# Optimization experiments

Measured on AMD Instinct MI355X. Metric: run time of the kernel, lower is better.

## Reference

```python
import jax, jax.numpy as jnp
import numpy as np
import math

D_MODEL = 1024
HEADS = 16
D_K = D_MODEL // HEADS
D_FF = 2048
EPS = 1e-6
NEG = -1e9


def _layernorm(x, gamma, beta):
    mu = x.mean(axis=-1, keepdims=True)
    var = ((x - mu) ** 2).mean(axis=-1, keepdims=True)
    return gamma * (x - mu) / jnp.sqrt(var + EPS) + beta


def setup_inputs() -> dict:
    key = jax.random.key(0)
    ks = jax.random.split(key, 12)
    B, S = 8, 1024
    s = 0.02
    return {
        "x": jax.random.normal(ks[0], (B, S, D_MODEL), jnp.float32),
        "mask": jnp.ones((B, 1, S), jnp.int32),
        "wq": jax.random.normal(ks[1], (D_MODEL, D_MODEL), jnp.float32) * s,
        "bq": jnp.zeros((D_MODEL,), jnp.float32),
        "wk": jax.random.normal(ks[2], (D_MODEL, D_MODEL), jnp.float32) * s,
        "bk": jnp.zeros((D_MODEL,), jnp.float32),
        "wv": jax.random.normal(ks[3], (D_MODEL, D_MODEL), jnp.float32) * s,
        "bv": jnp.zeros((D_MODEL,), jnp.float32),
        "wo": jax.random.normal(ks[4], (D_MODEL, D_MODEL), jnp.float32) * s,
        "bo": jnp.zeros((D_MODEL,), jnp.float32),
        "w1": jax.random.normal(ks[5], (D_MODEL, D_FF), jnp.float32) * s,
        "b1": jnp.zeros((D_FF,), jnp.float32),
        "w2": jax.random.normal(ks[6], (D_FF, D_MODEL), jnp.float32) * s,
        "b2": jnp.zeros((D_MODEL,), jnp.float32),
        "g1": jnp.ones((D_MODEL,), jnp.float32),
        "be1": jnp.zeros((D_MODEL,), jnp.float32),
        "g2": jnp.ones((D_MODEL,), jnp.float32),
        "be2": jnp.zeros((D_MODEL,), jnp.float32),
    }


def reference(x, mask, wq, bq, wk, bk, wv, bv, wo, bo, w1, b1, w2, b2, g1, be1, g2, be2):
    B, S, _ = x.shape
    # QKV projections, split heads: [B,H,S,d_k]
    q = (x @ wq + bq).reshape(B, S, HEADS, D_K).transpose(0, 2, 1, 3)
    k = (x @ wk + bk).reshape(B, S, HEADS, D_K).transpose(0, 2, 1, 3)
    v = (x @ wv + bv).reshape(B, S, HEADS, D_K).transpose(0, 2, 1, 3)
    scores = jnp.einsum("bhqd,bhkd->bhqk", q, k) / math.sqrt(D_K)
    m = mask[:, None, :, :]  # [B,1,1|S,S] broadcast over heads
    scores = jnp.where(m == 0, NEG, scores)
    attn = jax.nn.softmax(scores, axis=-1)
    out = jnp.einsum("bhqk,bhkd->bhqd", attn, v)
    concat = out.transpose(0, 2, 1, 3).reshape(B, S, D_MODEL)
    attn_out = concat @ wo + bo
    x1 = _layernorm(x + attn_out, g1, be1)
    ff = jax.nn.relu(x1 @ w1 + b1) @ w2 + b2
    return _layernorm(x1 + ff, g2, be2)
```

## Files before the change

kernel.cpp:

```cpp
#include <hip/hip_runtime.h>
#include <stdint.h>

using u16 = unsigned short;
using u32 = unsigned int;
typedef __attribute__((ext_vector_type(4))) float f32x4;
typedef __attribute__((ext_vector_type(8))) short s16x8;

#define LOG2E 1.44269504088896340736f
#define SCL (0.125f * LOG2E)

__device__ __forceinline__ u16 f2b(float f) {
  union { float f; u32 u; } v; v.f = f;
  u32 r = v.u + 0x7fffu + ((v.u >> 16) & 1u);
  return (u16)(r >> 16);
}

__device__ __forceinline__ float b2f(u16 x) {
  union { u32 u; float f; } v; v.u = (u32)x << 16; return v.f;
}

__device__ __forceinline__ u32 pack2(u16 lo, u16 hi) {
  return (u32)lo | ((u32)hi << 16);
}

__device__ __forceinline__ u32 cvtpk(float lo, float hi) {
  u32 r;
  asm("v_cvt_pk_bf16_f32 %0, %1, %2" : "=v"(r) : "v"(lo), "v"(hi));
  return r;
}

__device__ __forceinline__ float fexp2(float x) {
  float t = fmaf(x, 8388608.f, 1065053744.f);
  t = fmaxf(t, 0.f);
  union { u32 u; float f; } v; v.u = (u32)t;
  return v.f;
}

__device__ __forceinline__ f32x4 mfma16(s16x8 a, s16x8 b, f32x4 c) {
  return __builtin_amdgcn_mfma_f32_16x16x32_bf16(a, b, c, 0, 0, 0);
}

__device__ __forceinline__ void gload16(const void* g, void* l) {
  __builtin_amdgcn_global_load_lds(
      (const __attribute__((address_space(1))) void*)g,
      (__attribute__((address_space(3))) void*)l, 16, 0, 0);
}

__global__ __launch_bounds__(256) void cvt_bf16(const float* __restrict__ in,
                                                u16* __restrict__ out, int n4) {
  int i = blockIdx.x * 256 + threadIdx.x;
  if (i >= n4) return;
  float4 v = ((const float4*)in)[i];
  uint2 o;
  o.x = pack2(f2b(v.x), f2b(v.y));
  o.y = pack2(f2b(v.z), f2b(v.w));
  ((uint2*)out)[i] = o;
}

__global__ __launch_bounds__(256) void transpose_cvt(const float* __restrict__ in,
                                                     u16* __restrict__ outT,
                                                     int K, int N) {
  __shared__ float t[32][33];
  int n0 = blockIdx.x * 32, k0 = blockIdx.y * 32;
  int tx = threadIdx.x, ty = threadIdx.y;
#pragma unroll
  for (int i = 0; i < 4; i++)
    t[ty + i * 8][tx] = in[(size_t)(k0 + ty + i * 8) * N + n0 + tx];
  __syncthreads();
#pragma unroll
  for (int i = 0; i < 4; i++)
    outT[(size_t)(n0 + ty + i * 8) * K + k0 + tx] = f2b(t[tx][ty + i * 8]);
}

__global__ __launch_bounds__(256) void bias_pack(const float* __restrict__ bq,
                                                 const float* __restrict__ bk,
                                                 float* __restrict__ o) {
  int i = blockIdx.x * 256 + threadIdx.x;
  o[i] = (i < 1024) ? bq[i] : bk[i - 1024];
}

template <int EPI>
__global__ __launch_bounds__(512, 1) void gemmhk(const u16* __restrict__ A,
                                                 const u16* __restrict__ Bt,
                                                 const float* __restrict__ bias,
                                                 void* __restrict__ outp,
                                                 int N, int K) {
  __shared__ u16 As[2][2][128 * 64];
  __shared__ u16 Bs[2][2][128 * 64];
  int tid = threadIdx.x;
  int wv = tid >> 6, ln = tid & 63;
  int fr = ln & 15, fg = ln >> 4;
  int wm = wv >> 2, wn = wv & 3;

  int x = blockIdx.x & 7;
  int l = blockIdx.x >> 3;
  int m0 = (x * 4 + (l & 3)) * 256;
  int n0 = (l >> 2) * 256;

  const u16* Abase = A + (size_t)m0 * K;
  const u16* Bbase = Bt + (size_t)n0 * K;

  auto stageAq = [&](int buf, int h, int r0, int kt) {
    int row = tid >> 3, ch = tid & 7;
    int csw = ch ^ ((r0 + row) & 7);
    gload16(Abase + (size_t)(h * 128 + r0 + row) * K + kt * 64 + csw * 8,
            &As[buf][h][(size_t)(r0 * 8 + (wv << 6)) * 8]);
  };
  auto stageBh = [&](int buf, int h, int kt) {
#pragma unroll
    for (int s = 0; s < 2; s++) {
      int idx = s * 512 + tid;
      int row = idx >> 3, ch = idx & 7;
      int csw = ch ^ (row & 7);
      gload16(Bbase + (size_t)(h * 128 + row) * K + kt * 64 + csw * 8,
              &Bs[buf][h][(size_t)(s * 512 + (wv << 6)) * 8]);
    }
  };

  f32x4 acc[8][4] = {};
  int NT = K >> 6;

  stageAq(0, 0, 0, 0); stageAq(0, 1, 0, 0); stageBh(0, 0, 0);
  stageAq(0, 0, 64, 0); stageAq(0, 1, 64, 0); stageBh(0, 1, 0);

  for (int t = 0; t < NT; ++t) {
    int buf = t & 1, nbuf = buf ^ 1;
    int tn = (t + 1 < NT) ? t + 1 : t;
    const u16* Ah = &As[buf][wm][0];
    const u16* B0p = &Bs[buf][0][0];
    const u16* B1p = &Bs[buf][1][0];
    s16x8 a[4][2], b0[2][2], b1[2][2];

    asm volatile("s_waitcnt vmcnt(4)" ::: "memory");
    __builtin_amdgcn_s_barrier();
    __builtin_amdgcn_sched_barrier(0);
#pragma unroll
    for (int q = 0; q < 4; q++) {
      int row = q * 16 + fr;
#pragma unroll
      for (int ks = 0; ks < 2; ks++)
        a[q][ks] = *(const s16x8*)(Ah + row * 64 + (((ks * 4 + fg) ^ (row & 7)) << 3));
    }
#pragma unroll
    for (int pj = 0; pj < 2; pj++) {
      int row = wn * 32 + pj * 16 + fr;
#pragma unroll
      for (int ks = 0; ks < 2; ks++)
        b0[pj][ks] = *(const s16x8*)(B0p + row * 64 + (((ks * 4 + fg) ^ (row & 7)) << 3));
    }
    stageAq(nbuf, 0, 0, tn); stageAq(nbuf, 1, 0, tn); stageBh(nbuf, 0, tn);
    __builtin_amdgcn_sched_barrier(0);
    __builtin_amdgcn_s_setprio(1);
#pragma unroll
    for (int q = 0; q < 4; q++)
#pragma unroll
      for (int pj = 0; pj < 2; pj++) {
        acc[q][pj] = mfma16(a[q][0], b0[pj][0], acc[q][pj]);
        acc[q][pj] = mfma16(a[q][1], b0[pj][1], acc[q][pj]);
      }
    __builtin_amdgcn_s_setprio(0);
    __builtin_amdgcn_sched_barrier(0);

    asm volatile("s_waitcnt vmcnt(4)" ::: "memory");
    __builtin_amdgcn_s_barrier();
    __builtin_amdgcn_sched_barrier(0);
#pragma unroll
    for (int pj = 0; pj < 2; pj++) {
      int row = wn * 32 + pj * 16 + fr;
#pragma unroll
      for (int ks = 0; ks < 2; ks++)
        b1[pj][ks] = *(const s16x8*)(B1p + row * 64 + (((ks * 4 + fg) ^ (row & 7)) << 3));
    }
    stageAq(nbuf, 0, 64, tn); stageAq(nbuf, 1, 64, tn); stageBh(nbuf, 1, tn);
    __builtin_amdgcn_sched_barrier(0);
    __builtin_amdgcn_s_setprio(1);
#pragma unroll
    for (int q = 0; q < 4; q++)
#pragma unroll
      for (int pj = 0; pj < 2; pj++) {
        acc[q][2 + pj] = mfma16(a[q][0], b1[pj][0], acc[q][2 + pj]);
        acc[q][2 + pj] = mfma16(a[q][1], b1[pj][1], acc[q][2 + pj]);
      }
    __builtin_amdgcn_s_setprio(0);
    __builtin_amdgcn_sched_barrier(0);

#pragma unroll
    for (int q = 0; q < 4; q++) {
      int row = 64 + q * 16 + fr;
#pragma unroll
      for (int ks = 0; ks < 2; ks++)
        a[q][ks] = *(const s16x8*)(Ah + row * 64 + (((ks * 4 + fg) ^ (row & 7)) << 3));
    }
    __builtin_amdgcn_sched_barrier(0);
    __builtin_amdgcn_s_setprio(1);
#pragma unroll
    for (int q = 0; q < 4; q++)
#pragma unroll
      for (int pj = 0; pj < 2; pj++) {
        acc[4 + q][2 + pj] = mfma16(a[q][0], b1[pj][0], acc[4 + q][2 + pj]);
        acc[4 + q][2 + pj] = mfma16(a[q][1], b1[pj][1], acc[4 + q][2 + pj]);
      }
    __builtin_amdgcn_s_setprio(0);

    __builtin_amdgcn_s_setprio(1);
#pragma unroll
    for (int q = 0; q < 4; q++)
#pragma unroll
      for (int pj = 0; pj < 2; pj++) {
        acc[4 + q][pj] = mfma16(a[q][0], b0[pj][0], acc[4 + q][pj]);
        acc[4 + q][pj] = mfma16(a[q][1], b0[pj][1], acc[4 + q][pj]);
      }
    __builtin_amdgcn_s_setprio(0);
    __builtin_amdgcn_sched_barrier(0);
  }

#pragma unroll
  for (int j = 0; j < 4; j++) {
    int coll = n0 + (j >> 1) * 128 + wn * 32 + (j & 1) * 16 + fr;
    float bv = bias[coll];
#pragma unroll
    for (int i = 0; i < 8; i++) {
      int rowbase = m0 + wm * 128 + (i >> 2) * 64 + (i & 3) * 16 + fg * 4;
      if (EPI == 5) {
        u16* o = (u16*)outp + (size_t)(coll >> 10) * (8192u * 1024u) + (coll & 1023);
#pragma unroll
        for (int r = 0; r < 4; r++)
          o[(size_t)(rowbase + r) * 1024] = f2b(acc[i][j][r] + bv);
      } else {
#pragma unroll
        for (int r = 0; r < 4; r++) {
          float v = acc[i][j][r] + bv;
          if (EPI == 2) v = v > 0.f ? v : 0.f;
          ((u16*)outp)[(size_t)(rowbase + r) * N + coll] = f2b(v);
        }
      }
    }
  }
}

template <int EPI, int BN, int WM, int WN>
__global__ __launch_bounds__(512, 1) void gemm8(const u16* __restrict__ A,
                                                const u16* __restrict__ Bt,
                                                const float* __restrict__ bias,
                                                void* __restrict__ outp,
                                                int N, int K) {
  constexpr int MI = 256 / (WM * 16);
  constexpr int NJ = BN / (WN * 16);
  constexpr int BB = BN / 128;
  __shared__ u16 As[4][256 * 32];
  __shared__ u16 Bs[4][BN * 32];
  int tid = threadIdx.x;
  int wv = tid >> 6, ln = tid & 63;
  int fr = ln & 15, fg = ln >> 4;
  int wm = wv / WN, wn = wv % WN;

  int x = blockIdx.x & 7;
  int l = blockIdx.x >> 3;
  int m0 = (x * 4 + (l & 3)) * 256;
  int n0 = (l >> 2) * BN;

  auto stageA = [&](int buf, int kt) {
#pragma unroll
    for (int s = 0; s < 2; s++) {
      int idx = s * 512 + tid;
      int row = idx >> 2, ch = idx & 3;
      int sw = (row ^ (row >> 2)) & 3;
      int gcol = kt * 32 + ((ch ^ sw) << 3);
      gload16(A + (size_t)(m0 + row) * K + gcol,
              &As[buf][(size_t)(s * 512 + (wv << 6)) * 8]);
    }
  };
  auto stageB = [&](int buf, int kt) {
#pragma unroll
    for (int s = 0; s < BB; s++) {
      int idx = s * 512 + tid;
      int row = idx >> 2, ch = idx & 3;
      int sw = (row ^ (row >> 2)) & 3;
      int gcol = kt * 32 + ((ch ^ sw) << 3);
      gload16(Bt + (size_t)(n0 + row) * K + gcol,
              &Bs[buf][(size_t)(s * 512 + (wv << 6)) * 8]);
    }
  };

  f32x4 acc[MI][NJ] = {};
  int NT = K >> 5;

#pragma unroll
  for (int tt = 0; tt < 3; ++tt) { stageA(tt, tt); stageB(tt, tt); }

  for (int t = 0; t < NT; ++t) {
    if constexpr (BN == 256) asm volatile("s_waitcnt vmcnt(8)" ::: "memory");
    else                     asm volatile("s_waitcnt vmcnt(6)" ::: "memory");
    __builtin_amdgcn_s_barrier();
    __builtin_amdgcn_sched_barrier(0);

    const u16* Ab = As[t & 3];
    const u16* Bb = Bs[t & 3];
    s16x8 af[MI], bf[NJ];
#pragma unroll
    for (int j = 0; j < NJ; j++) {
      int row = wn * (BN / WN) + j * 16 + fr;
      int sw = (row ^ (row >> 2)) & 3;
      bf[j] = *(const s16x8*)&Bb[row * 32 + ((fg ^ sw) << 3)];
    }
#pragma unroll
    for (int i = 0; i < MI; i++) {
      int row = wm * (256 / WM) + i * 16 + fr;
      int sw = (row ^ (row >> 2)) & 3;
      af[i] = *(const s16x8*)&Ab[row * 32 + ((fg ^ sw) << 3)];
    }

    int tn = (t + 3 < NT) ? t + 3 : NT - 1;
    stageA((t + 3) & 3, tn);
    stageB((t + 3) & 3, tn);

    __builtin_amdgcn_sched_barrier(0);
    __builtin_amdgcn_s_setprio(1);
#pragma unroll
    for (int i = 0; i < MI; i++)
#pragma unroll
      for (int j = 0; j < NJ; j++)
        acc[i][j] = mfma16(af[i], bf[j], acc[i][j]);
    __builtin_amdgcn_s_setprio(0);
    __builtin_amdgcn_sched_barrier(0);
  }

#pragma unroll
  for (int j = 0; j < NJ; j++) {
    int coll = n0 + wn * (BN / WN) + j * 16 + fr;
    float bv = bias[coll];
#pragma unroll
    for (int i = 0; i < MI; i++) {
      int rowbase = m0 + wm * (256 / WM) + i * 16 + fg * 4;
      if (EPI == 3) {
        int b_ = rowbase >> 10, s_ = rowbase & 1023;
        int h_ = coll >> 6, d_ = coll & 63;
        float v0 = acc[i][j][0] + bv, v1 = acc[i][j][1] + bv;
        float v2 = acc[i][j][2] + bv, v3 = acc[i][j][3] + bv;
        uint2 o; o.x = pack2(f2b(v0), f2b(v1)); o.y = pack2(f2b(v2), f2b(v3));
        *(uint2*)((u16*)outp + (((size_t)((b_ * 16 + h_) * 64 + d_)) << 10) + s_) = o;
      } else {
#pragma unroll
        for (int r = 0; r < 4; r++) {
          int row = rowbase + r;
          float v = acc[i][j][r] + bv;
          ((u16*)outp)[(size_t)row * N + coll] = f2b(v);
        }
      }
    }
  }
}

__global__ __launch_bounds__(256) void attn_fwd(const u16* __restrict__ q,
                                                const u16* __restrict__ k,
                                                const u16* __restrict__ vT,
                                                const int* __restrict__ mask,
                                                u16* __restrict__ ctx) {
  __shared__ u16 Ks[64 * 64];
  __shared__ u16 Vs[2][64 * 64];
  __shared__ u16 Ps[4][32 * 64];
  int tid = threadIdx.x, wv = tid >> 6, ln = tid & 63;
  int fr = ln & 15, fg = ln >> 4;
  int bh = blockIdx.x, b = bh >> 4, h = bh & 15;
  int q0 = blockIdx.y * 128;

  const u16* kbase = k + (size_t)b * 1024 * 1024 + h * 64;
  const u16* vbase = vT + (size_t)bh * 64 * 1024;

  int cl0 = wv * 64 + ln, cl1 = cl0 + 256;
  int rr0 = cl0 >> 3, csw0 = (cl0 & 7) ^ (rr0 & 7);
  int rr1 = cl1 >> 3, csw1 = (cl1 & 7) ^ (rr1 & 7);
  const u16* kc0 = kbase + rr0 * 1024 + csw0 * 8;
  const u16* kc1 = kbase + rr1 * 1024 + csw1 * 8;
  const u16* vc0 = vbase + rr0 * 1024 + csw0 * 8;
  const u16* vc1 = vbase + rr1 * 1024 + csw1 * 8;
  u16* Kd0 = Ks + (size_t)(wv * 64) * 8;
  u16* Kd1 = Kd0 + 256 * 8;

  gload16(kc0, Kd0); gload16(kc1, Kd1);
  gload16(vc0, Vs[0] + (size_t)(wv * 64) * 8);
  gload16(vc1, Vs[0] + (size_t)(wv * 64 + 256) * 8);
  kc0 += 65536; kc1 += 65536; vc0 += 64; vc1 += 64;

  int okm = 1;
#pragma unroll
  for (int t4 = 0; t4 < 4; t4++) {
    int4 mv = ((const int4*)(mask + b * 1024))[ln * 4 + t4];
    okm &= (mv.x != 0) & (mv.y != 0) & (mv.z != 0) & (mv.w != 0);
  }
  int seq_ok = __all(okm);

  s16x8 qf[2][2];
#pragma unroll
  for (int i = 0; i < 2; i++)
#pragma unroll
    for (int ks = 0; ks < 2; ks++) {
      int row = q0 + wv * 32 + i * 16 + fr;
      qf[i][ks] = *(const s16x8*)(q + (size_t)(b * 1024 + row) * 1024 + h * 64 + ks * 32 + fg * 8);
      u32* qw = (u32*)&qf[i][ks];
#pragma unroll
      for (int w = 0; w < 4; w++) {
        union { u32 u; float f; } lo, hi;
        lo.u = qw[w] << 16; hi.u = qw[w] & 0xffff0000u;
        qw[w] = cvtpk(lo.f * SCL, hi.f * SCL);
      }
    }

  s16x8 ones;
#pragma unroll
  for (int j = 0; j < 8; j++) ones[j] = (short)0x3F80;

  f32x4 ao[2][4] = {};
  f32x4 aol[2] = {};

  __syncthreads();

  for (int kt = 0; kt < 16; ++kt) {
    int cur = kt & 1;

    f32x4 st[4][2] = {};
    __builtin_amdgcn_s_setprio(1);
#pragma unroll
    for (int ks = 0; ks < 2; ks++)
#pragma unroll
      for (int jm = 0; jm < 4; jm++) {
        s16x8 kfr = *(const s16x8*)(Ks + (jm * 16 + fr) * 64 + (((ks * 4 + fg) ^ (fr & 7)) << 3));
        st[jm][0] = mfma16(kfr, qf[0][ks], st[jm][0]);
        st[jm][1] = mfma16(kfr, qf[1][ks], st[jm][1]);
      }
    __builtin_amdgcn_s_setprio(0);

    __syncthreads();
    if (kt < 15) {
      u16* Vd = Vs[cur ^ 1];
      gload16(kc0, Kd0); gload16(kc1, Kd1);
      gload16(vc0, Vd + (size_t)(wv * 64) * 8);
      gload16(vc1, Vd + (size_t)(wv * 64 + 256) * 8);
      kc0 += 65536; kc1 += 65536; vc0 += 64; vc1 += 64;
    }

    if (!seq_ok) {
#pragma unroll
      for (int jm = 0; jm < 4; jm++) {
        int4 mv = *(const int4*)(mask + b * 1024 + kt * 64 + jm * 16 + fg * 4);
        float m0 = mv.x == 0 ? -1e9f * SCL : 0.f;
        float m1 = mv.y == 0 ? -1e9f * SCL : 0.f;
        float m2 = mv.z == 0 ? -1e9f * SCL : 0.f;
        float m3 = mv.w == 0 ? -1e9f * SCL : 0.f;
#pragma unroll
        for (int i = 0; i < 2; i++) {
          st[jm][i][0] += m0; st[jm][i][1] += m1;
          st[jm][i][2] += m2; st[jm][i][3] += m3;
        }
      }
    }

#pragma unroll
    for (int i = 0; i < 2; i++)
#pragma unroll
      for (int jm = 0; jm < 4; jm++)
#pragma unroll
        for (int r = 0; r < 4; r++)
          st[jm][i][r] = fexp2(st[jm][i][r]);

    u16* Pw = Ps[wv];
#pragma unroll
    for (int i = 0; i < 2; i++) {
      int qrow = i * 16 + fr;
      int rowoff = qrow * 64;
      int sw = (qrow & 7) << 3;
#pragma unroll
      for (int jm = 0; jm < 4; jm++) {
        uint2 pk;
        pk.x = cvtpk(st[jm][i][0], st[jm][i][1]);
        pk.y = cvtpk(st[jm][i][2], st[jm][i][3]);
        *(uint2*)(Pw + ((rowoff + jm * 16 + fg * 4) ^ sw)) = pk;
      }
    }

    const u16* Vc = Vs[cur];
    __builtin_amdgcn_s_setprio(1);
#pragma unroll
    for (int ks = 0; ks < 2; ks++) {
      int ch = ((ks * 4 + fg) ^ (fr & 7)) << 3;
      s16x8 pa0 = *(const s16x8*)(Pw + fr * 64 + ch);
      s16x8 pa1 = *(const s16x8*)(Pw + (16 + fr) * 64 + ch);
#pragma unroll
      for (int jd = 0; jd < 4; jd++) {
        s16x8 bv = *(const s16x8*)(Vc + (jd * 16 + fr) * 64 + ch);
        ao[0][jd] = mfma16(pa0, bv, ao[0][jd]);
        ao[1][jd] = mfma16(pa1, bv, ao[1][jd]);
      }
      aol[0] = mfma16(pa0, ones, aol[0]);
      aol[1] = mfma16(pa1, ones, aol[1]);
    }
    __builtin_amdgcn_s_setprio(0);

    __syncthreads();
  }

#pragma unroll
  for (int io = 0; io < 2; io++) {
    float i0 = 1.f / aol[io][0], i1 = 1.f / aol[io][1];
    float i2 = 1.f / aol[io][2], i3 = 1.f / aol[io][3];
#pragma unroll
    for (int jd = 0; jd < 4; jd++) {
      int d = jd * 16 + fr;
      int rowb = wv * 32 + io * 16 + fg * 4;
      u16* cb = ctx + (size_t)(b * 1024 + q0 + rowb) * 1024 + h * 64 + d;
      cb[0]    = f2b(ao[io][jd][0] * i0);
      cb[1024] = f2b(ao[io][jd][1] * i1);
      cb[2048] = f2b(ao[io][jd][2] * i2);
      cb[3072] = f2b(ao[io][jd][3] * i3);
    }
  }
}

template <bool ABF16, bool BBF16>
__global__ __launch_bounds__(256) void ln_fused(const void* __restrict__ a,
                                                const void* __restrict__ bsrc,
                                                const float* __restrict__ gamma,
                                                const float* __restrict__ beta,
                                                float* __restrict__ outf,
                                                u16* __restrict__ outb) {
  int row = blockIdx.x, tid = threadIdx.x;
  float v0, v1, v2, v3;
  if (ABF16) {
    uint2 va = ((const uint2*)((const u16*)a + (size_t)row * 1024))[tid];
    v0 = b2f((u16)(va.x & 0xffff)); v1 = b2f((u16)(va.x >> 16));
    v2 = b2f((u16)(va.y & 0xffff)); v3 = b2f((u16)(va.y >> 16));
  } else {
    float4 va = ((const float4*)((const float*)a + (size_t)row * 1024))[tid];
    v0 = va.x; v1 = va.y; v2 = va.z; v3 = va.w;
  }
  if (BBF16) {
    uint2 vb = ((const uint2*)((const u16*)bsrc + (size_t)row * 1024))[tid];
    v0 += b2f((u16)(vb.x & 0xffff)); v1 += b2f((u16)(vb.x >> 16));
    v2 += b2f((u16)(vb.y & 0xffff)); v3 += b2f((u16)(vb.y >> 16));
  } else {
    float4 vb = ((const float4*)((const float*)bsrc + (size_t)row * 1024))[tid];
    v0 += vb.x; v1 += vb.y; v2 += vb.z; v3 += vb.w;
  }
  float s = v0 + v1 + v2 + v3;
  float ss = v0 * v0 + v1 * v1 + v2 * v2 + v3 * v3;
#pragma unroll
  for (int m = 1; m < 64; m <<= 1) { s += __shfl_xor(s, m); ss += __shfl_xor(ss, m); }
  __shared__ float rs[8];
  int wv = tid >> 6;
  if ((tid & 63) == 0) { rs[wv] = s; rs[4 + wv] = ss; }
  __syncthreads();
  s = rs[0] + rs[1] + rs[2] + rs[3];
  ss = rs[4] + rs[5] + rs[6] + rs[7];
  float mu = s * (1.f / 1024.f);
  float var = ss * (1.f / 1024.f) - mu * mu;
  float rstd = rsqrtf(var + 1e-6f);
  float4 g4 = ((const float4*)gamma)[tid];
  float4 be4 = ((const float4*)beta)[tid];
  float y0 = g4.x * (v0 - mu) * rstd + be4.x;
  float y1 = g4.y * (v1 - mu) * rstd + be4.y;
  float y2 = g4.z * (v2 - mu) * rstd + be4.z;
  float y3 = g4.w * (v3 - mu) * rstd + be4.w;
  if (outf) {
    float4 o; o.x = y0; o.y = y1; o.z = y2; o.w = y3;
    ((float4*)(outf + (size_t)row * 1024))[tid] = o;
  }
  if (outb) {
    uint2 ob; ob.x = pack2(f2b(y0), f2b(y1)); ob.y = pack2(f2b(y2), f2b(y3));
    ((uint2*)(outb + (size_t)row * 1024))[tid] = ob;
  }
}

extern "C" void kernel_launch(void* const* d_in, const int* in_sizes, int n_in,
                              void* d_out, int out_size, void* d_ws, size_t ws_size,
                              hipStream_t stream) {
  const float* x   = (const float*)d_in[0];
  const int*   msk = (const int*)d_in[1];
  const float* wq  = (const float*)d_in[2];
  const float* bq  = (const float*)d_in[3];
  const float* wk  = (const float*)d_in[4];
  const float* bk  = (const float*)d_in[5];
  const float* wv  = (const float*)d_in[6];
  const float* bv  = (const float*)d_in[7];
  const float* wo  = (const float*)d_in[8];
  const float* bo  = (const float*)d_in[9];
  const float* w1  = (const float*)d_in[10];
  const float* b1  = (const float*)d_in[11];
  const float* w2  = (const float*)d_in[12];
  const float* b2  = (const float*)d_in[13];
  const float* g1  = (const float*)d_in[14];
  const float* be1 = (const float*)d_in[15];
  const float* g2  = (const float*)d_in[16];
  const float* be2 = (const float*)d_in[17];
  float* out = (float*)d_out;
  char* ws = (char*)d_ws;
  const size_t MB = 1u << 20;

  u16* xb  = (u16*)(ws + 0);
  u16* wqt = (u16*)(ws + 16 * MB);
  u16* wkt = (u16*)(ws + 18 * MB);
  u16* wvt = (u16*)(ws + 20 * MB);
  u16* wot = (u16*)(ws + 22 * MB);
  u16* w1t = (u16*)(ws + 24 * MB);
  u16* w2t = (u16*)(ws + 28 * MB);
  u16* qb  = (u16*)(ws + 32 * MB);
  u16* kb  = (u16*)(ws + 48 * MB);
  u16* vT  = (u16*)(ws + 64 * MB);
  u16* ctx = (u16*)(ws + 80 * MB);
  float* bqk = (float*)(ws + 80 * MB);
  u16* attn_out = (u16*)(ws + 32 * MB);
  u16* x1b = (u16*)(ws + 0);
  u16* hb  = (u16*)(ws + 96 * MB);
  u16* fff = (u16*)(ws + 48 * MB);

  dim3 tb(32, 8);
  cvt_bf16<<<8192, 256, 0, stream>>>(x, xb, 8192 * 1024 / 4);
  transpose_cvt<<<dim3(32, 32), tb, 0, stream>>>(wq, wqt, 1024, 1024);
  transpose_cvt<<<dim3(32, 32), tb, 0, stream>>>(wk, wkt, 1024, 1024);
  transpose_cvt<<<dim3(32, 32), tb, 0, stream>>>(wv, wvt, 1024, 1024);
  transpose_cvt<<<dim3(32, 32), tb, 0, stream>>>(wo, wot, 1024, 1024);
  transpose_cvt<<<dim3(64, 32), tb, 0, stream>>>(w1, w1t, 1024, 2048);
  transpose_cvt<<<dim3(32, 64), tb, 0, stream>>>(w2, w2t, 2048, 1024);
  bias_pack<<<8, 256, 0, stream>>>(bq, bk, bqk);

  gemmhk<5><<<256, 512, 0, stream>>>(xb, wqt, bqk, qb, 2048, 1024);
  gemm8<3, 128, 4, 2><<<256, 512, 0, stream>>>(xb, wvt, bv, vT, 1024, 1024);

  attn_fwd<<<dim3(128, 8), 256, 0, stream>>>(qb, kb, vT, msk, ctx);

  gemm8<0, 128, 4, 2><<<256, 512, 0, stream>>>(ctx, wot, bo, attn_out, 1024, 1024);
  ln_fused<true, true><<<8192, 256, 0, stream>>>(xb, attn_out, g1, be1, nullptr, x1b);
  gemmhk<2><<<256, 512, 0, stream>>>(x1b, w1t, b1, hb, 2048, 1024);
  gemm8<0, 128, 4, 2><<<256, 512, 0, stream>>>(hb, w2t, b2, fff, 1024, 2048);
  ln_fused<true, true><<<8192, 256, 0, stream>>>(x1b, fff, g2, be2, out, nullptr);
}
```

Measured before the change: 261.9 us.

## Load K and V fragments directly from global memory in attention, dropping LDS staging

```diff
diff --git a/kernel.cpp b/kernel.cpp
--- a/kernel.cpp
+++ b/kernel.cpp
@@ -356,8 +356,6 @@
                                                 const u16* __restrict__ vT,
                                                 const int* __restrict__ mask,
                                                 u16* __restrict__ ctx) {
-  __shared__ u16 Ks[64 * 64];
-  __shared__ u16 Vs[2][64 * 64];
   __shared__ u16 Ps[4][32 * 64];
   int tid = threadIdx.x, wv = tid >> 6, ln = tid & 63;
   int fr = ln & 15, fg = ln >> 4;
@@ -367,20 +365,14 @@
   const u16* kbase = k + (size_t)b * 1024 * 1024 + h * 64;
   const u16* vbase = vT + (size_t)bh * 64 * 1024;
 
-  int cl0 = wv * 64 + ln, cl1 = cl0 + 256;
-  int rr0 = cl0 >> 3, csw0 = (cl0 & 7) ^ (rr0 & 7);
-  int rr1 = cl1 >> 3, csw1 = (cl1 & 7) ^ (rr1 & 7);
-  const u16* kc0 = kbase + rr0 * 1024 + csw0 * 8;
-  const u16* kc1 = kbase + rr1 * 1024 + csw1 * 8;
-  const u16* vc0 = vbase + rr0 * 1024 + csw0 * 8;
-  const u16* vc1 = vbase + rr1 * 1024 + csw1 * 8;
-  u16* Kd0 = Ks + (size_t)(wv * 64) * 8;
-  u16* Kd1 = Kd0 + 256 * 8;
-
-  gload16(kc0, Kd0); gload16(kc1, Kd1);
-  gload16(vc0, Vs[0] + (size_t)(wv * 64) * 8);
-  gload16(vc1, Vs[0] + (size_t)(wv * 64 + 256) * 8);
-  kc0 += 65536; kc1 += 65536; vc0 += 64; vc1 += 64;
+  const u16* kp0 = kbase + (0 * 16 + fr) * 1024 + fg * 8;
+  const u16* kp1 = kbase + (1 * 16 + fr) * 1024 + fg * 8;
+  const u16* kp2 = kbase + (2 * 16 + fr) * 1024 + fg * 8;
+  const u16* kp3 = kbase + (3 * 16 + fr) * 1024 + fg * 8;
+  const u16* vp0 = vbase + (0 * 16 + fr) * 1024 + fg * 8;
+  const u16* vp1 = vbase + (1 * 16 + fr) * 1024 + fg * 8;
+  const u16* vp2 = vbase + (2 * 16 + fr) * 1024 + fg * 8;
+  const u16* vp3 = vbase + (3 * 16 + fr) * 1024 + fg * 8;
 
   int okm = 1;
 #pragma unroll
@@ -412,11 +404,17 @@
 
   f32x4 ao[2][4] = {};
   f32x4 aol[2] = {};
-
-  __syncthreads();
+  u16* Pw = Ps[wv];
 
   for (int kt = 0; kt < 16; ++kt) {
-    int cur = kt & 1;
+    s16x8 kf[2][4];
+#pragma unroll
+    for (int ks = 0; ks < 2; ks++) {
+      kf[ks][0] = *(const s16x8*)(kp0 + ks * 32);
+      kf[ks][1] = *(const s16x8*)(kp1 + ks * 32);
+      kf[ks][2] = *(const s16x8*)(kp2 + ks * 32);
+      kf[ks][3] = *(const s16x8*)(kp3 + ks * 32);
+    }
 
     f32x4 st[4][2] = {};
     __builtin_amdgcn_s_setprio(1);
@@ -424,20 +422,10 @@
     for (int ks = 0; ks < 2; ks++)
 #pragma unroll
       for (int jm = 0; jm < 4; jm++) {
-        s16x8 kfr = *(const s16x8*)(Ks + (jm * 16 + fr) * 64 + (((ks * 4 + fg) ^ (fr & 7)) << 3));
-        st[jm][0] = mfma16(kfr, qf[0][ks], st[jm][0]);
-        st[jm][1] = mfma16(kfr, qf[1][ks], st[jm][1]);
+        st[jm][0] = mfma16(kf[ks][jm], qf[0][ks], st[jm][0]);
+        st[jm][1] = mfma16(kf[ks][jm], qf[1][ks], st[jm][1]);
       }
     __builtin_amdgcn_s_setprio(0);
-
-    __syncthreads();
-    if (kt < 15) {
-      u16* Vd = Vs[cur ^ 1];
-      gload16(kc0, Kd0); gload16(kc1, Kd1);
-      gload16(vc0, Vd + (size_t)(wv * 64) * 8);
-      gload16(vc1, Vd + (size_t)(wv * 64 + 256) * 8);
-      kc0 += 65536; kc1 += 65536; vc0 += 64; vc1 += 64;
-    }
 
     if (!seq_ok) {
 #pragma unroll
@@ -463,7 +451,6 @@
         for (int r = 0; r < 4; r++)
           st[jm][i][r] = fexp2(st[jm][i][r]);
 
-    u16* Pw = Ps[wv];
 #pragma unroll
     for (int i = 0; i < 2; i++) {
       int qrow = i * 16 + fr;
@@ -478,25 +465,30 @@
       }
     }
 
-    const u16* Vc = Vs[cur];
     __builtin_amdgcn_s_setprio(1);
 #pragma unroll
     for (int ks = 0; ks < 2; ks++) {
       int ch = ((ks * 4 + fg) ^ (fr & 7)) << 3;
       s16x8 pa0 = *(const s16x8*)(Pw + fr * 64 + ch);
       s16x8 pa1 = *(const s16x8*)(Pw + (16 + fr) * 64 + ch);
-#pragma unroll
-      for (int jd = 0; jd < 4; jd++) {
-        s16x8 bv = *(const s16x8*)(Vc + (jd * 16 + fr) * 64 + ch);
-        ao[0][jd] = mfma16(pa0, bv, ao[0][jd]);
-        ao[1][jd] = mfma16(pa1, bv, ao[1][jd]);
-      }
+      s16x8 bv0 = *(const s16x8*)(vp0 + kt * 64 + ks * 32);
+      s16x8 bv1 = *(const s16x8*)(vp1 + kt * 64 + ks * 32);
+      s16x8 bv2 = *(const s16x8*)(vp2 + kt * 64 + ks * 32);
+      s16x8 bv3 = *(const s16x8*)(vp3 + kt * 64 + ks * 32);
+      ao[0][0] = mfma16(pa0, bv0, ao[0][0]);
+      ao[1][0] = mfma16(pa1, bv0, ao[1][0]);
+      ao[0][1] = mfma16(pa0, bv1, ao[0][1]);
+      ao[1][1] = mfma16(pa1, bv1, ao[1][1]);
+      ao[0][2] = mfma16(pa0, bv2, ao[0][2]);
+      ao[1][2] = mfma16(pa1, bv2, ao[1][2]);
+      ao[0][3] = mfma16(pa0, bv3, ao[0][3]);
+      ao[1][3] = mfma16(pa1, bv3, ao[1][3]);
       aol[0] = mfma16(pa0, ones, aol[0]);
       aol[1] = mfma16(pa1, ones, aol[1]);
     }
     __builtin_amdgcn_s_setprio(0);
 
-    __syncthreads();
+    kp0 += 65536; kp1 += 65536; kp2 += 65536; kp3 += 65536;
   }
 
 #pragma unroll
```

Measured after the change: 352.9 us. 1.35x slower.

## Restage GEMM loads into four interleaved quarter-tile phases with barriers

Applied to the files above, without the earlier changes.

```diff
diff --git a/kernel.cpp b/kernel.cpp
--- a/kernel.cpp
+++ b/kernel.cpp
@@ -100,28 +100,24 @@
   const u16* Abase = A + (size_t)m0 * K;
   const u16* Bbase = Bt + (size_t)n0 * K;
 
-  auto stageAq = [&](int buf, int h, int r0, int kt) {
-    int row = tid >> 3, ch = tid & 7;
-    int csw = ch ^ ((r0 + row) & 7);
-    gload16(Abase + (size_t)(h * 128 + r0 + row) * K + kt * 64 + csw * 8,
-            &As[buf][h][(size_t)(r0 * 8 + (wv << 6)) * 8]);
-  };
-  auto stageBh = [&](int buf, int h, int kt) {
-#pragma unroll
-    for (int s = 0; s < 2; s++) {
-      int idx = s * 512 + tid;
+  auto stage = [&](const u16* gbase, u16* lbase, int kt) {
+#pragma unroll
+    for (int rnd = 0; rnd < 2; rnd++) {
+      int idx = rnd * 512 + tid;
       int row = idx >> 3, ch = idx & 7;
       int csw = ch ^ (row & 7);
-      gload16(Bbase + (size_t)(h * 128 + row) * K + kt * 64 + csw * 8,
-              &Bs[buf][h][(size_t)(s * 512 + (wv << 6)) * 8]);
+      gload16(gbase + (size_t)row * K + kt * 64 + csw * 8,
+              lbase + (size_t)(rnd * 512 + (wv << 6)) * 8);
     }
   };
 
   f32x4 acc[8][4] = {};
   int NT = K >> 6;
 
-  stageAq(0, 0, 0, 0); stageAq(0, 1, 0, 0); stageBh(0, 0, 0);
-  stageAq(0, 0, 64, 0); stageAq(0, 1, 64, 0); stageBh(0, 1, 0);
+  stage(Abase, &As[0][0][0], 0);
+  stage(Abase + (size_t)128 * K, &As[0][1][0], 0);
+  stage(Bbase, &Bs[0][0][0], 0);
+  stage(Bbase + (size_t)128 * K, &Bs[0][1][0], 0);
 
   for (int t = 0; t < NT; ++t) {
     int buf = t & 1, nbuf = buf ^ 1;
@@ -131,7 +127,8 @@
     const u16* B1p = &Bs[buf][1][0];
     s16x8 a[4][2], b0[2][2], b1[2][2];
 
-    asm volatile("s_waitcnt vmcnt(4)" ::: "memory");
+    stage(Abase, &As[nbuf][0][0], tn);
+    asm volatile("s_waitcnt vmcnt(2)" ::: "memory");
     __builtin_amdgcn_s_barrier();
     __builtin_amdgcn_sched_barrier(0);
 #pragma unroll
@@ -148,8 +145,6 @@
       for (int ks = 0; ks < 2; ks++)
         b0[pj][ks] = *(const s16x8*)(B0p + row * 64 + (((ks * 4 + fg) ^ (row & 7)) << 3));
     }
-    stageAq(nbuf, 0, 0, tn); stageAq(nbuf, 1, 0, tn); stageBh(nbuf, 0, tn);
-    __builtin_amdgcn_sched_barrier(0);
     __builtin_amdgcn_s_setprio(1);
 #pragma unroll
     for (int q = 0; q < 4; q++)
@@ -161,7 +156,7 @@
     __builtin_amdgcn_s_setprio(0);
     __builtin_amdgcn_sched_barrier(0);
 
-    asm volatile("s_waitcnt vmcnt(4)" ::: "memory");
+    stage(Abase + (size_t)128 * K, &As[nbuf][1][0], tn);
     __builtin_amdgcn_s_barrier();
     __builtin_amdgcn_sched_barrier(0);
 #pragma unroll
@@ -171,8 +166,6 @@
       for (int ks = 0; ks < 2; ks++)
         b1[pj][ks] = *(const s16x8*)(B1p + row * 64 + (((ks * 4 + fg) ^ (row & 7)) << 3));
     }
-    stageAq(nbuf, 0, 64, tn); stageAq(nbuf, 1, 64, tn); stageBh(nbuf, 1, tn);
-    __builtin_amdgcn_sched_barrier(0);
     __builtin_amdgcn_s_setprio(1);
 #pragma unroll
     for (int q = 0; q < 4; q++)
@@ -184,6 +177,9 @@
     __builtin_amdgcn_s_setprio(0);
     __builtin_amdgcn_sched_barrier(0);
 
+    stage(Bbase, &Bs[nbuf][0][0], tn);
+    __builtin_amdgcn_s_barrier();
+    __builtin_amdgcn_sched_barrier(0);
 #pragma unroll
     for (int q = 0; q < 4; q++) {
       int row = 64 + q * 16 + fr;
@@ -191,7 +187,6 @@
       for (int ks = 0; ks < 2; ks++)
         a[q][ks] = *(const s16x8*)(Ah + row * 64 + (((ks * 4 + fg) ^ (row & 7)) << 3));
     }
-    __builtin_amdgcn_sched_barrier(0);
     __builtin_amdgcn_s_setprio(1);
 #pragma unroll
     for (int q = 0; q < 4; q++)
@@ -201,7 +196,11 @@
         acc[4 + q][2 + pj] = mfma16(a[q][1], b1[pj][1], acc[4 + q][2 + pj]);
       }
     __builtin_amdgcn_s_setprio(0);
-
+    __builtin_amdgcn_sched_barrier(0);
+
+    stage(Bbase + (size_t)128 * K, &Bs[nbuf][1][0], tn);
+    __builtin_amdgcn_s_barrier();
+    __builtin_amdgcn_sched_barrier(0);
     __builtin_amdgcn_s_setprio(1);
 #pragma unroll
     for (int q = 0; q < 4; q++)
@@ -412,6 +411,7 @@
 
   f32x4 ao[2][4] = {};
   f32x4 aol[2] = {};
+  u16* Pw = Ps[wv];
 
   __syncthreads();
 
@@ -463,7 +463,6 @@
         for (int r = 0; r < 4; r++)
           st[jm][i][r] = fexp2(st[jm][i][r]);
 
-    u16* Pw = Ps[wv];
 #pragma unroll
     for (int i = 0; i < 2; i++) {
       int qrow = i * 16 + fr;
```

After: 266.4 us. No clear change (+1.7%).
